# Optimization experiments

Measured on AMD Instinct MI355X. Metric: run time of the kernel, lower is better.

Reference implementation:

```python
import jax, jax.numpy as jnp
import numpy as np

B, T, C, H = 4, 2048, 1024, 16
D = C // H          # head_dim = 64
FF = 2 * C          # ff_mult = 2
EPS = 1e-5


def _layernorm(x, g, b):
    mu = jnp.mean(x, axis=-1, keepdims=True)
    var = jnp.mean((x - mu) ** 2, axis=-1, keepdims=True)
    return (x - mu) * jax.lax.rsqrt(var + EPS) * g + b


def setup_inputs() -> dict:
    key = jax.random.key(0)
    ks = jax.random.split(key, 8)
    x = jax.random.normal(ks[0], (B, T, C), dtype=jnp.float32)
    perm = jax.random.permutation(ks[1], T).astype(jnp.int32)
    s_c = 1.0 / np.sqrt(C)
    s_f = 1.0 / np.sqrt(FF)
    Wqkv = jax.random.normal(ks[2], (C, 3 * C), dtype=jnp.float32) * s_c
    Wproj = jax.random.normal(ks[3], (C, C), dtype=jnp.float32) * s_c
    bproj = jnp.zeros((C,), dtype=jnp.float32)
    ln1_g = jnp.ones((C,), dtype=jnp.float32)
    ln1_b = jnp.zeros((C,), dtype=jnp.float32)
    ln2_g = jnp.ones((C,), dtype=jnp.float32)
    ln2_b = jnp.zeros((C,), dtype=jnp.float32)
    Wff1 = jax.random.normal(ks[4], (C, FF), dtype=jnp.float32) * s_c
    bff1 = jnp.zeros((FF,), dtype=jnp.float32)
    Wff2 = jax.random.normal(ks[5], (FF, C), dtype=jnp.float32) * s_f
    bff2 = jnp.zeros((C,), dtype=jnp.float32)
    return {"x": x, "perm": perm, "Wqkv": Wqkv, "Wproj": Wproj, "bproj": bproj,
            "ln1_g": ln1_g, "ln1_b": ln1_b, "ln2_g": ln2_g, "ln2_b": ln2_b,
            "Wff1": Wff1, "bff1": bff1, "Wff2": Wff2, "bff2": bff2}


def reference(x, perm, Wqkv, Wproj, bproj, ln1_g, ln1_b, ln2_g, ln2_b,
              Wff1, bff1, Wff2, bff2):
    # --- attention branch ---
    h = _layernorm(x, ln1_g, ln1_b)                       # [B,T,C]
    qkv = (h @ Wqkv).reshape(B, T, 3, H, D)
    q, k, v = qkv[:, :, 0], qkv[:, :, 1], qkv[:, :, 2]    # [B,T,H,D]
    # random-permuted causal additive mask: masked = ~tril[:, perm]
    rows = jnp.arange(T)[:, None]
    masked = perm[None, :] > rows                          # [T,T] bool
    bias = jnp.where(masked, -jnp.inf, 0.0).astype(x.dtype)
    scale = 1.0 / np.sqrt(D)
    scores = jnp.einsum('bqhd,bkhd->bhqk', q, k) * scale + bias
    attn = jax.nn.softmax(scores, axis=-1)                 # [B,H,T,T]
    y = jnp.einsum('bhqk,bkhd->bqhd', attn, v).reshape(B, T, C)
    x = x + y @ Wproj + bproj
    # --- MLP branch ---
    h2 = _layernorm(x, ln2_g, ln2_b)
    ff = jax.nn.gelu(h2 @ Wff1 + bff1, approximate=False) @ Wff2 + bff2
    return x + ff
```

## Files before the change

### kernel.cpp

```cpp
#include <hip/hip_runtime.h>
#include <math.h>

#define Bb 4
#define Tt 2048
#define Cc 1024
#define Hh 16
#define Dd 64
#define FFf 2048
#define Mrows (Bb*Tt)

typedef _Float16 f16;
typedef _Float16 half8 __attribute__((ext_vector_type(8)));
typedef _Float16 half4 __attribute__((ext_vector_type(4)));
typedef _Float16 half2 __attribute__((ext_vector_type(2)));
typedef float floatx4 __attribute__((ext_vector_type(4)));
typedef float floatx16 __attribute__((ext_vector_type(16)));

#define MFMA16(a,b,c)    __builtin_amdgcn_mfma_f32_16x16x32_f16(a,b,c,0,0,0)
#define MFMA16K16(a,b,c) __builtin_amdgcn_mfma_f32_16x16x16f16(a,b,c,0,0,0)
#define MFMA32(a,b,c)    __builtin_amdgcn_mfma_f32_32x32x16_f16(a,b,c,0,0,0)

__device__ __forceinline__ void g2l16(const void* g, void* l) {
  __builtin_amdgcn_global_load_lds((__attribute__((address_space(1))) void*)(g),
                                   (__attribute__((address_space(3))) void*)(l),
                                   16, 0, 0);
}

__global__ __launch_bounds__(256) void wt_all_kernel(
    const float* __restrict__ Wqkv, const float* __restrict__ Wproj,
    const float* __restrict__ Wff1, const float* __restrict__ Wff2,
    f16* __restrict__ WqkvT, f16* __restrict__ WprojT,
    f16* __restrict__ Wff1T, f16* __restrict__ Wff2T) {
  __shared__ float tile[32][33];
  int idx = blockIdx.x;
  const float* W; f16* WT; int K, N, n0, k0;
  if (idx < 3072)      { W = Wqkv;  WT = WqkvT;  K = Cc;  N = 3*Cc; n0 = (idx % 96)*32; k0 = (idx / 96)*32; }
  else if (idx < 4096) { idx -= 3072; W = Wproj; WT = WprojT; K = Cc;  N = Cc;  n0 = (idx % 32)*32; k0 = (idx / 32)*32; }
  else if (idx < 6144) { idx -= 4096; W = Wff1;  WT = Wff1T;  K = Cc;  N = FFf; n0 = (idx % 64)*32; k0 = (idx / 64)*32; }
  else                 { idx -= 6144; W = Wff2;  WT = Wff2T;  K = FFf; N = Cc;  n0 = (idx % 32)*32; k0 = (idx / 32)*32; }
  const int tx = threadIdx.x, ty = threadIdx.y;
  #pragma unroll
  for (int i = 0; i < 4; i++)
    tile[ty + 8*i][tx] = W[(size_t)(k0 + ty + 8*i) * N + n0 + tx];
  __syncthreads();
  #pragma unroll
  for (int i = 0; i < 4; i++)
    WT[(size_t)(n0 + ty + 8*i) * K + k0 + tx] = (f16)tile[tx][ty + 8*i];
}

__global__ __launch_bounds__(256) void ln_kernel(const float* __restrict__ x,
                                                 const float* __restrict__ gam,
                                                 const float* __restrict__ bet,
                                                 f16* __restrict__ out) {
  const int row = blockIdx.x;
  const int tid = threadIdx.x;
  const float4 v = ((const float4*)(x + (size_t)row * Cc))[tid];
  float s  = v.x + v.y + v.z + v.w;
  float ss = v.x*v.x + v.y*v.y + v.z*v.z + v.w*v.w;
  #pragma unroll
  for (int o = 32; o >= 1; o >>= 1) { s += __shfl_xor(s, o); ss += __shfl_xor(ss, o); }
  __shared__ float ps[4], pss[4];
  if ((tid & 63) == 0) { ps[tid >> 6] = s; pss[tid >> 6] = ss; }
  __syncthreads();
  s  = ps[0] + ps[1] + ps[2] + ps[3];
  ss = pss[0] + pss[1] + pss[2] + pss[3];
  const float mu   = s * (1.0f / Cc);
  const float rstd = rsqrtf(ss * (1.0f / Cc) - mu * mu + 1e-5f);
  const float4 g4 = ((const float4*)gam)[tid];
  const float4 b4 = ((const float4*)bet)[tid];
  half4 o;
  o[0] = (f16)((v.x - mu) * rstd * g4.x + b4.x);
  o[1] = (f16)((v.y - mu) * rstd * g4.y + b4.y);
  o[2] = (f16)((v.z - mu) * rstd * g4.z + b4.z);
  o[3] = (f16)((v.w - mu) * rstd * g4.w + b4.w);
  ((half4*)(out + (size_t)row * Cc))[tid] = o;
}

template <int MODE>
__global__ __launch_bounds__(256, 3) void gemm_kernel(
    const f16* __restrict__ A, const f16* __restrict__ Bt, const int Kdim,
    const float* __restrict__ resid, const float* __restrict__ bias,
    float* __restrict__ outF, f16* __restrict__ outH,
    f16* __restrict__ outQ, f16* __restrict__ outK, f16* __restrict__ outV) {
  __shared__ f16 As[128 * 64];
  __shared__ f16 Bs[128 * 64];
  const int tid = threadIdx.x;
  const int lane = tid & 63;
  const int w = tid >> 6;
  const int wr = w >> 1, wc = w & 1;
  const int bm = blockIdx.y, bn = blockIdx.x;

  floatx16 acc[2][2] = {};

  const int srow = lane >> 3;
  const int scol = ((lane & 7) ^ srow) * 8;
  const size_t aBase = (size_t)(bm*128 + w*32 + srow) * Kdim + scol;
  const size_t bBase = (size_t)(bn*128 + w*32 + srow) * Kdim + scol;

  const int m0 = wr*64 + (lane & 31);
  const int n0 = wc*64 + (lane & 31);
  const int khalf = lane >> 5;
  const int mx = (lane & 7);

  for (int ks = 0; ks < Kdim; ks += 64) {
    __syncthreads();
    #pragma unroll
    for (int c = 0; c < 4; c++) {
      g2l16(A  + aBase + (size_t)(c*8)*Kdim + ks, &As[(w*32 + c*8) * 64]);
      g2l16(Bt + bBase + (size_t)(c*8)*Kdim + ks, &Bs[(w*32 + c*8) * 64]);
    }
    __syncthreads();
    #pragma unroll
    for (int kk = 0; kk < 4; kk++) {
      const int kg = kk*2 + khalf;
      half8 aF[2], bF[2];
      aF[0] = *(const half8*)&As[(m0     ) * 64 + ((kg ^ mx) * 8)];
      aF[1] = *(const half8*)&As[(m0 + 32) * 64 + ((kg ^ mx) * 8)];
      bF[0] = *(const half8*)&Bs[(n0     ) * 64 + ((kg ^ mx) * 8)];
      bF[1] = *(const half8*)&Bs[(n0 + 32) * 64 + ((kg ^ mx) * 8)];
      acc[0][0] = MFMA32(aF[0], bF[0], acc[0][0]);
      acc[0][1] = MFMA32(aF[0], bF[1], acc[0][1]);
      acc[1][0] = MFMA32(aF[1], bF[0], acc[1][0]);
      acc[1][1] = MFMA32(aF[1], bF[1], acc[1][1]);
    }
  }

  const int rowBase = bm*128 + wr*64;
  const int colBase = bn*128 + wc*64;
  #pragma unroll
  for (int mi = 0; mi < 2; mi++) {
    #pragma unroll
    for (int ni = 0; ni < 2; ni++) {
      const int col = colBase + ni*32 + (lane & 31);
      if (MODE == 0) {
        const int s = col >> 10;
        const int hh = (col >> 6) & 15;
        const int d = col & 63;
        #pragma unroll
        for (int g = 0; g < 4; g++) {
          const int row0 = rowBase + mi*32 + 4*khalf + 8*g;
          const int bI = row0 >> 11;
          const int t0 = row0 & 2047;
          if (s == 2) {
            const size_t addr = (((size_t)(bI*Hh + hh)) * Dd + d) * Tt +
                                (t0 & ~63) + ((t0 >> 2) & 3)*16 + ((t0 >> 4) & 3)*4;
            half4 o;
            #pragma unroll
            for (int r = 0; r < 4; r++) o[r] = (f16)acc[mi][ni][g*4 + r];
            *(half4*)&outV[addr] = o;
          } else {
            f16* dst = (s == 0) ? outQ : outK;
            const float sc = (s == 0) ? 0.18033688f : 1.0f;
            #pragma unroll
            for (int r = 0; r < 4; r++)
              dst[(((size_t)(bI*Hh + hh)) * Tt + t0 + r) * Dd + d] =
                  (f16)(acc[mi][ni][g*4 + r] * sc);
          }
        }
      } else {
        #pragma unroll
        for (int g = 0; g < 4; g++) {
          #pragma unroll
          for (int r = 0; r < 4; r++) {
            const int row = rowBase + mi*32 + 4*khalf + 8*g + r;
            const float vv = acc[mi][ni][g*4 + r];
            if (MODE == 1) {
              const size_t a = (size_t)row * Cc + col;
              outF[a] = vv + resid[a] + bias[col];
            } else if (MODE == 2) {
              const float t = vv + bias[col];
              const float gl = 0.5f * t * (1.0f + erff(t * 0.70710678118654752f));
              outH[(size_t)row * FFf + col] = (f16)gl;
            } else {
              const size_t a = (size_t)row * Cc + col;
              outF[a] = vv + bias[col] + resid[a];
            }
          }
        }
      }
    }
  }
}

__global__ __launch_bounds__(256, 4) void attn_kernel(
    const f16* __restrict__ Q, const f16* __restrict__ Kg,
    const f16* __restrict__ Vtp, const int* __restrict__ perm,
    f16* __restrict__ Y) {
  __shared__ f16 Ks[64 * 64];
  __shared__ f16 Vs[64 * 64];
  __shared__ int permS[64];

  const int tid = threadIdx.x;
  const int lane = tid & 63;
  const int w = tid >> 6;
  const int low = lane & 15;
  const int quad = lane >> 4;
  const int bh = blockIdx.y;
  const int q0 = blockIdx.x * 128;
  const int b = bh >> 4, h = bh & 15;

  half8 qF[2][2];
  {
    const size_t base = ((size_t)bh * Tt + q0 + w*32) * Dd;
    #pragma unroll
    for (int qi = 0; qi < 2; qi++)
      #pragma unroll
      for (int kc = 0; kc < 2; kc++)
        qF[qi][kc] = *(const half8*)(Q + base + (size_t)(qi*16 + low) * Dd +
                                     kc*32 + quad*8);
  }

  floatx4 O[4][2] = {};
  floatx4 Ol[2] = {};
  const half4 ones4 = {(f16)1.f, (f16)1.f, (f16)1.f, (f16)1.f};

  const int gd = ((lane & 7) ^ (lane >> 3)) * 8;
  const int krow = lane >> 3;

  for (int kt = 0; kt < Tt / 64; kt++) {
    const int kbase = kt * 64;
    __syncthreads();
    {
      const size_t kgBase = ((size_t)bh * Tt + kbase) * Dd;
      const size_t vgBase = ((size_t)bh * Dd) * Tt + kbase;
      g2l16(Kg  + kgBase + (size_t)(w*16 + 0 + krow) * Dd + gd, &Ks[(w*2 + 0) * 512]);
      g2l16(Kg  + kgBase + (size_t)(w*16 + 8 + krow) * Dd + gd, &Ks[(w*2 + 1) * 512]);
      g2l16(Vtp + vgBase + (size_t)(w*16 + 0 + krow) * Tt + gd, &Vs[(w*2 + 0) * 512]);
      g2l16(Vtp + vgBase + (size_t)(w*16 + 8 + krow) * Tt + gd, &Vs[(w*2 + 1) * 512]);
      if (tid < 64) permS[tid] = perm[kbase + tid];
    }
    __syncthreads();

    floatx4 S[2][4] = {};
    #pragma unroll
    for (int kc = 0; kc < 2; kc++) {
      #pragma unroll
      for (int ki = 0; ki < 4; ki++) {
        const int key = ki*16 + low;
        const half8 kf = *(const half8*)&Ks[key * 64 + (((kc*4 + quad) ^ (lane & 7)) * 8)];
        S[0][ki] = MFMA16(kf, qF[0][kc], S[0][ki]);
        S[1][ki] = MFMA16(kf, qF[1][kc], S[1][ki]);
      }
    }

    int4 pk[4];
    #pragma unroll
    for (int ki = 0; ki < 4; ki++) pk[ki] = *(const int4*)&permS[ki*16 + quad*4];

    half4 pF[2][4];
    #pragma unroll
    for (int qi = 0; qi < 2; qi++) {
      const int qrow = q0 + w*32 + qi*16 + low;
      #pragma unroll
      for (int ki = 0; ki < 4; ki++) {
        const floatx4 sv = S[qi][ki];
        const float p0 = (pk[ki].x > qrow) ? 0.f : __builtin_amdgcn_exp2f(sv[0]);
        const float p1 = (pk[ki].y > qrow) ? 0.f : __builtin_amdgcn_exp2f(sv[1]);
        const float p2 = (pk[ki].z > qrow) ? 0.f : __builtin_amdgcn_exp2f(sv[2]);
        const float p3 = (pk[ki].w > qrow) ? 0.f : __builtin_amdgcn_exp2f(sv[3]);
        const half2 lo = __builtin_bit_cast(half2, __builtin_amdgcn_cvt_pkrtz(p0, p1));
        const half2 hi = __builtin_bit_cast(half2, __builtin_amdgcn_cvt_pkrtz(p2, p3));
        pF[qi][ki] = __builtin_shufflevector(lo, hi, 0, 1, 2, 3);
      }
    }

    #pragma unroll
    for (int ki2 = 0; ki2 < 2; ki2++) {
      Ol[0] = MFMA16K16(ones4, pF[0][2*ki2 + 0], Ol[0]);
      Ol[1] = MFMA16K16(ones4, pF[1][2*ki2 + 0], Ol[1]);
      Ol[0] = MFMA16K16(ones4, pF[0][2*ki2 + 1], Ol[0]);
      Ol[1] = MFMA16K16(ones4, pF[1][2*ki2 + 1], Ol[1]);
      #pragma unroll
      for (int ni = 0; ni < 4; ni++) {
        const int d = ni*16 + low;
        const half8 v8 = *(const half8*)&Vs[d * 64 + (((quad*2 + ki2) ^ (lane & 7)) * 8)];
        const half4 vfA = __builtin_shufflevector(v8, v8, 0, 1, 2, 3);
        const half4 vfB = __builtin_shufflevector(v8, v8, 4, 5, 6, 7);
        O[ni][0] = MFMA16K16(vfA, pF[0][2*ki2 + 0], O[ni][0]);
        O[ni][1] = MFMA16K16(vfA, pF[1][2*ki2 + 0], O[ni][1]);
        O[ni][0] = MFMA16K16(vfB, pF[0][2*ki2 + 1], O[ni][0]);
        O[ni][1] = MFMA16K16(vfB, pF[1][2*ki2 + 1], O[ni][1]);
      }
    }
  }

  #pragma unroll
  for (int qi = 0; qi < 2; qi++) {
    const float linv = 1.0f / Ol[qi][0];
    const int trow = q0 + w*32 + qi*16 + low;
    #pragma unroll
    for (int ni = 0; ni < 4; ni++) {
      half4 o;
      #pragma unroll
      for (int r = 0; r < 4; r++) o[r] = (f16)(O[ni][qi][r] * linv);
      *(half4*)&Y[((size_t)(b * Tt + trow)) * Cc + h*64 + ni*16 + quad*4] = o;
    }
  }
}

extern "C" void kernel_launch(void* const* d_in, const int* in_sizes, int n_in,
                              void* d_out, int out_size, void* d_ws, size_t ws_size,
                              hipStream_t stream) {
  const float* x     = (const float*)d_in[0];
  const int*   perm  = (const int*)d_in[1];
  const float* Wqkv  = (const float*)d_in[2];
  const float* Wproj = (const float*)d_in[3];
  const float* bproj = (const float*)d_in[4];
  const float* ln1g  = (const float*)d_in[5];
  const float* ln1b  = (const float*)d_in[6];
  const float* ln2g  = (const float*)d_in[7];
  const float* ln2b  = (const float*)d_in[8];
  const float* Wff1  = (const float*)d_in[9];
  const float* bff1  = (const float*)d_in[10];
  const float* Wff2  = (const float*)d_in[11];
  const float* bff2  = (const float*)d_in[12];
  float* out = (float*)d_out;

  char* ws = (char*)d_ws;
  size_t off = 0;
  auto alloc = [&](size_t bytes) -> void* {
    void* p = ws + off;
    off += (bytes + 255) & ~(size_t)255;
    return p;
  };
  f16*   h1     = (f16*)alloc((size_t)Mrows * Cc * 2);
  f16*   qb     = (f16*)alloc((size_t)Mrows * Cc * 2);
  f16*   kb     = (f16*)alloc((size_t)Mrows * Cc * 2);
  f16*   vtp    = (f16*)alloc((size_t)Mrows * Cc * 2);
  f16*   yb     = (f16*)alloc((size_t)Mrows * Cc * 2);
  float* xa     = (float*)alloc((size_t)Mrows * Cc * 4);
  f16*   h2     = (f16*)alloc((size_t)Mrows * Cc * 2);
  f16*   gb     = (f16*)alloc((size_t)Mrows * FFf * 2);
  f16*   WqkvT  = (f16*)alloc((size_t)3 * Cc * Cc * 2);
  f16*   WprojT = (f16*)alloc((size_t)Cc * Cc * 2);
  f16*   Wff1T  = (f16*)alloc((size_t)FFf * Cc * 2);
  f16*   Wff2T  = (f16*)alloc((size_t)Cc * FFf * 2);

  wt_all_kernel<<<8192, dim3(32, 8), 0, stream>>>(Wqkv, Wproj, Wff1, Wff2,
                                                  WqkvT, WprojT, Wff1T, Wff2T);

  ln_kernel<<<Mrows, 256, 0, stream>>>(x, ln1g, ln1b, h1);

  gemm_kernel<0><<<dim3(3*Cc/128, Mrows/128), 256, 0, stream>>>(
      h1, WqkvT, Cc, nullptr, nullptr, nullptr, nullptr, qb, kb, vtp);

  attn_kernel<<<dim3(Tt/128, Bb*Hh), 256, 0, stream>>>(qb, kb, vtp, perm, yb);

  gemm_kernel<1><<<dim3(Cc/128, Mrows/128), 256, 0, stream>>>(
      yb, WprojT, Cc, x, bproj, xa, nullptr, nullptr, nullptr, nullptr);

  ln_kernel<<<Mrows, 256, 0, stream>>>(xa, ln2g, ln2b, h2);

  gemm_kernel<2><<<dim3(FFf/128, Mrows/128), 256, 0, stream>>>(
      h2, Wff1T, Cc, nullptr, bff1, nullptr, gb, nullptr, nullptr, nullptr);

  gemm_kernel<3><<<dim3(Cc/128, Mrows/128), 256, 0, stream>>>(
      gb, Wff2T, FFf, xa, bff2, out, nullptr, nullptr, nullptr, nullptr);
}
```

Before: 446.4 us.

## Double-buffer attention K/V tiles and raise GEMM occupancy bound

The attention kernel now keeps two LDS buffers for the K, V and perm tiles. It issues the async global-to-LDS load for the next key tile before computing on the current one, so each iteration needs one barrier instead of two and the load latency overlaps the MFMA work. The GEMM launch bound goes from 3 to 4 blocks per CU, and its epilogue moves into a separate inline helper. The costs are twice the LDS per attention block and tighter register limits on the GEMM, which could cause spills.

```diff
diff --git a/kernel.cpp b/kernel.cpp
--- a/kernel.cpp
+++ b/kernel.cpp
@@ -77,7 +77,60 @@
 }
 
 template <int MODE>
-__global__ __launch_bounds__(256, 3) void gemm_kernel(
+__device__ __forceinline__ void gemm_epilogue_tile(
+    const floatx16& a, int rowBase, int col, int khalf,
+    const float* __restrict__ resid, const float* __restrict__ bias,
+    float* __restrict__ outF, f16* __restrict__ outH,
+    f16* __restrict__ outQ, f16* __restrict__ outK, f16* __restrict__ outV) {
+  if (MODE == 0) {
+    const int s = col >> 10;
+    const int hh = (col >> 6) & 15;
+    const int d = col & 63;
+    #pragma unroll
+    for (int g = 0; g < 4; g++) {
+      const int row0 = rowBase + 4*khalf + 8*g;
+      const int bI = row0 >> 11;
+      const int t0 = row0 & 2047;
+      if (s == 2) {
+        const size_t addr = (((size_t)(bI*Hh + hh)) * Dd + d) * Tt +
+                            (t0 & ~63) + ((t0 >> 2) & 3)*16 + ((t0 >> 4) & 3)*4;
+        half4 o;
+        #pragma unroll
+        for (int r = 0; r < 4; r++) o[r] = (f16)a[g*4 + r];
+        *(half4*)&outV[addr] = o;
+      } else {
+        f16* dst = (s == 0) ? outQ : outK;
+        const float sc = (s == 0) ? 0.18033688f : 1.0f;
+        #pragma unroll
+        for (int r = 0; r < 4; r++)
+          dst[(((size_t)(bI*Hh + hh)) * Tt + t0 + r) * Dd + d] = (f16)(a[g*4 + r] * sc);
+      }
+    }
+  } else {
+    #pragma unroll
+    for (int g = 0; g < 4; g++) {
+      #pragma unroll
+      for (int r = 0; r < 4; r++) {
+        const int row = rowBase + 4*khalf + 8*g + r;
+        const float vv = a[g*4 + r];
+        if (MODE == 1) {
+          const size_t ad = (size_t)row * Cc + col;
+          outF[ad] = vv + resid[ad] + bias[col];
+        } else if (MODE == 2) {
+          const float t = vv + bias[col];
+          const float gl = 0.5f * t * (1.0f + erff(t * 0.70710678118654752f));
+          outH[(size_t)row * FFf + col] = (f16)gl;
+        } else {
+          const size_t ad = (size_t)row * Cc + col;
+          outF[ad] = vv + bias[col] + resid[ad];
+        }
+      }
+    }
+  }
+}
+
+template <int MODE>
+__global__ __launch_bounds__(256, 4) void gemm_kernel(
     const f16* __restrict__ A, const f16* __restrict__ Bt, const int Kdim,
     const float* __restrict__ resid, const float* __restrict__ bias,
     float* __restrict__ outF, f16* __restrict__ outH,
@@ -125,70 +178,22 @@
     }
   }
 
-  const int rowBase = bm*128 + wr*64;
-  const int colBase = bn*128 + wc*64;
-  #pragma unroll
-  for (int mi = 0; mi < 2; mi++) {
-    #pragma unroll
-    for (int ni = 0; ni < 2; ni++) {
-      const int col = colBase + ni*32 + (lane & 31);
-      if (MODE == 0) {
-        const int s = col >> 10;
-        const int hh = (col >> 6) & 15;
-        const int d = col & 63;
-        #pragma unroll
-        for (int g = 0; g < 4; g++) {
-          const int row0 = rowBase + mi*32 + 4*khalf + 8*g;
-          const int bI = row0 >> 11;
-          const int t0 = row0 & 2047;
-          if (s == 2) {
-            const size_t addr = (((size_t)(bI*Hh + hh)) * Dd + d) * Tt +
-                                (t0 & ~63) + ((t0 >> 2) & 3)*16 + ((t0 >> 4) & 3)*4;
-            half4 o;
-            #pragma unroll
-            for (int r = 0; r < 4; r++) o[r] = (f16)acc[mi][ni][g*4 + r];
-            *(half4*)&outV[addr] = o;
-          } else {
-            f16* dst = (s == 0) ? outQ : outK;
-            const float sc = (s == 0) ? 0.18033688f : 1.0f;
-            #pragma unroll
-            for (int r = 0; r < 4; r++)
-              dst[(((size_t)(bI*Hh + hh)) * Tt + t0 + r) * Dd + d] =
-                  (f16)(acc[mi][ni][g*4 + r] * sc);
-          }
-        }
-      } else {
-        #pragma unroll
-        for (int g = 0; g < 4; g++) {
-          #pragma unroll
-          for (int r = 0; r < 4; r++) {
-            const int row = rowBase + mi*32 + 4*khalf + 8*g + r;
-            const float vv = acc[mi][ni][g*4 + r];
-            if (MODE == 1) {
-              const size_t a = (size_t)row * Cc + col;
-              outF[a] = vv + resid[a] + bias[col];
-            } else if (MODE == 2) {
-              const float t = vv + bias[col];
-              const float gl = 0.5f * t * (1.0f + erff(t * 0.70710678118654752f));
-              outH[(size_t)row * FFf + col] = (f16)gl;
-            } else {
-              const size_t a = (size_t)row * Cc + col;
-              outF[a] = vv + bias[col] + resid[a];
-            }
-          }
-        }
-      }
-    }
-  }
+  #pragma unroll
+  for (int mi = 0; mi < 2; mi++)
+    #pragma unroll
+    for (int ni = 0; ni < 2; ni++)
+      gemm_epilogue_tile<MODE>(acc[mi][ni], blockIdx.y*128 + wr*64 + mi*32,
+                               blockIdx.x*128 + wc*64 + ni*32 + (lane & 31), khalf,
+                               resid, bias, outF, outH, outQ, outK, outV);
 }
 
 __global__ __launch_bounds__(256, 4) void attn_kernel(
     const f16* __restrict__ Q, const f16* __restrict__ Kg,
     const f16* __restrict__ Vtp, const int* __restrict__ perm,
     f16* __restrict__ Y) {
-  __shared__ f16 Ks[64 * 64];
-  __shared__ f16 Vs[64 * 64];
-  __shared__ int permS[64];
+  __shared__ f16 Ks[2 * 4096];
+  __shared__ f16 Vs[2 * 4096];
+  __shared__ int permS[2 * 64];
 
   const int tid = threadIdx.x;
   const int lane = tid & 63;
@@ -199,6 +204,21 @@
   const int q0 = blockIdx.x * 128;
   const int b = bh >> 4, h = bh & 15;
 
+  const int gd = ((lane & 7) ^ (lane >> 3)) * 8;
+  const int krow = lane >> 3;
+
+  const size_t kgBase0 = (size_t)bh * Tt * Dd;
+  const size_t vgBase0 = (size_t)bh * Dd * Tt;
+
+  auto stage = [&](int kt, int bufi) {
+    const int kbase = kt * 64;
+    g2l16(Kg  + kgBase0 + (size_t)(kbase + w*16 + 0 + krow) * Dd + gd, &Ks[bufi*4096 + (w*2 + 0) * 512]);
+    g2l16(Kg  + kgBase0 + (size_t)(kbase + w*16 + 8 + krow) * Dd + gd, &Ks[bufi*4096 + (w*2 + 1) * 512]);
+    g2l16(Vtp + vgBase0 + (size_t)(w*16 + 0 + krow) * Tt + kbase + gd, &Vs[bufi*4096 + (w*2 + 0) * 512]);
+    g2l16(Vtp + vgBase0 + (size_t)(w*16 + 8 + krow) * Tt + kbase + gd, &Vs[bufi*4096 + (w*2 + 1) * 512]);
+    if (tid < 64) permS[bufi*64 + tid] = perm[kbase + tid];
+  };
+
   half8 qF[2][2];
   {
     const size_t base = ((size_t)bh * Tt + q0 + w*32) * Dd;
@@ -214,22 +234,16 @@
   floatx4 Ol[2] = {};
   const half4 ones4 = {(f16)1.f, (f16)1.f, (f16)1.f, (f16)1.f};
 
-  const int gd = ((lane & 7) ^ (lane >> 3)) * 8;
-  const int krow = lane >> 3;
+  stage(0, 0);
 
   for (int kt = 0; kt < Tt / 64; kt++) {
-    const int kbase = kt * 64;
+    const int cur = kt & 1;
     __syncthreads();
-    {
-      const size_t kgBase = ((size_t)bh * Tt + kbase) * Dd;
-      const size_t vgBase = ((size_t)bh * Dd) * Tt + kbase;
-      g2l16(Kg  + kgBase + (size_t)(w*16 + 0 + krow) * Dd + gd, &Ks[(w*2 + 0) * 512]);
-      g2l16(Kg  + kgBase + (size_t)(w*16 + 8 + krow) * Dd + gd, &Ks[(w*2 + 1) * 512]);
-      g2l16(Vtp + vgBase + (size_t)(w*16 + 0 + krow) * Tt + gd, &Vs[(w*2 + 0) * 512]);
-      g2l16(Vtp + vgBase + (size_t)(w*16 + 8 + krow) * Tt + gd, &Vs[(w*2 + 1) * 512]);
-      if (tid < 64) permS[tid] = perm[kbase + tid];
-    }
-    __syncthreads();
+    if (kt + 1 < Tt / 64) stage(kt + 1, cur ^ 1);
+
+    const f16* KsH = &Ks[cur * 4096];
+    const f16* VsH = &Vs[cur * 4096];
+    const int* pS  = &permS[cur * 64];
 
     floatx4 S[2][4] = {};
     #pragma unroll
@@ -237,7 +251,7 @@
       #pragma unroll
       for (int ki = 0; ki < 4; ki++) {
         const int key = ki*16 + low;
-        const half8 kf = *(const half8*)&Ks[key * 64 + (((kc*4 + quad) ^ (lane & 7)) * 8)];
+        const half8 kf = *(const half8*)&KsH[key * 64 + (((kc*4 + quad) ^ (lane & 7)) * 8)];
         S[0][ki] = MFMA16(kf, qF[0][kc], S[0][ki]);
         S[1][ki] = MFMA16(kf, qF[1][kc], S[1][ki]);
       }
@@ -245,7 +259,7 @@
 
     int4 pk[4];
     #pragma unroll
-    for (int ki = 0; ki < 4; ki++) pk[ki] = *(const int4*)&permS[ki*16 + quad*4];
+    for (int ki = 0; ki < 4; ki++) pk[ki] = *(const int4*)&pS[ki*16 + quad*4];
 
     half4 pF[2][4];
     #pragma unroll
@@ -273,7 +287,7 @@
       #pragma unroll
       for (int ni = 0; ni < 4; ni++) {
         const int d = ni*16 + low;
-        const half8 v8 = *(const half8*)&Vs[d * 64 + (((quad*2 + ki2) ^ (lane & 7)) * 8)];
+        const half8 v8 = *(const half8*)&VsH[d * 64 + (((quad*2 + ki2) ^ (lane & 7)) * 8)];
         const half4 vfA = __builtin_shufflevector(v8, v8, 0, 1, 2, 3);
         const half4 vfB = __builtin_shufflevector(v8, v8, 4, 5, 6, 7);
         O[ni][0] = MFMA16K16(vfA, pF[0][2*ki2 + 0], O[ni][0]);
```

Result: no change. 448.4 us (+0.4%).

## Merge weight transpose with LN1, remap GEMM blocks per XCD, raise occupancy

Applied to the files above, without the earlier changes.

Folds the weight transpose/convert kernel and the first layernorm into a single launch, removing one kernel boundary. GEMM blocks are remapped so that each XCD (selected by fid&7) handles a fixed set of column tiles, which should improve L2 reuse of the B operand within each XCD. The GEMM launch bound is also raised from 3 to 4 waves, which may increase register pressure. The epilogue is moved into a helper without changing its behaviour.

```diff
diff --git a/kernel.cpp b/kernel.cpp
--- a/kernel.cpp
+++ b/kernel.cpp
@@ -26,26 +26,53 @@
                                    16, 0, 0);
 }
 
-__global__ __launch_bounds__(256) void wt_all_kernel(
+__global__ __launch_bounds__(256) void wt_ln_kernel(
     const float* __restrict__ Wqkv, const float* __restrict__ Wproj,
     const float* __restrict__ Wff1, const float* __restrict__ Wff2,
     f16* __restrict__ WqkvT, f16* __restrict__ WprojT,
-    f16* __restrict__ Wff1T, f16* __restrict__ Wff2T) {
-  __shared__ float tile[32][33];
-  int idx = blockIdx.x;
-  const float* W; f16* WT; int K, N, n0, k0;
-  if (idx < 3072)      { W = Wqkv;  WT = WqkvT;  K = Cc;  N = 3*Cc; n0 = (idx % 96)*32; k0 = (idx / 96)*32; }
-  else if (idx < 4096) { idx -= 3072; W = Wproj; WT = WprojT; K = Cc;  N = Cc;  n0 = (idx % 32)*32; k0 = (idx / 32)*32; }
-  else if (idx < 6144) { idx -= 4096; W = Wff1;  WT = Wff1T;  K = Cc;  N = FFf; n0 = (idx % 64)*32; k0 = (idx / 64)*32; }
-  else                 { idx -= 6144; W = Wff2;  WT = Wff2T;  K = FFf; N = Cc;  n0 = (idx % 32)*32; k0 = (idx / 32)*32; }
-  const int tx = threadIdx.x, ty = threadIdx.y;
-  #pragma unroll
-  for (int i = 0; i < 4; i++)
-    tile[ty + 8*i][tx] = W[(size_t)(k0 + ty + 8*i) * N + n0 + tx];
-  __syncthreads();
-  #pragma unroll
-  for (int i = 0; i < 4; i++)
-    WT[(size_t)(n0 + ty + 8*i) * K + k0 + tx] = (f16)tile[tx][ty + 8*i];
+    f16* __restrict__ Wff1T, f16* __restrict__ Wff2T,
+    const float* __restrict__ x, const float* __restrict__ gam,
+    const float* __restrict__ bet, f16* __restrict__ lnout) {
+  const int tid = threadIdx.x;
+  if (blockIdx.x < 8192) {
+    __shared__ float tile[32][33];
+    int idx = blockIdx.x;
+    const float* W; f16* WT; int K, N, n0, k0;
+    if (idx < 3072)      { W = Wqkv;  WT = WqkvT;  K = Cc;  N = 3*Cc; n0 = (idx % 96)*32; k0 = (idx / 96)*32; }
+    else if (idx < 4096) { idx -= 3072; W = Wproj; WT = WprojT; K = Cc;  N = Cc;  n0 = (idx % 32)*32; k0 = (idx / 32)*32; }
+    else if (idx < 6144) { idx -= 4096; W = Wff1;  WT = Wff1T;  K = Cc;  N = FFf; n0 = (idx % 64)*32; k0 = (idx / 64)*32; }
+    else                 { idx -= 6144; W = Wff2;  WT = Wff2T;  K = FFf; N = Cc;  n0 = (idx % 32)*32; k0 = (idx / 32)*32; }
+    const int tx = tid & 31, ty = tid >> 5;
+    #pragma unroll
+    for (int i = 0; i < 4; i++)
+      tile[ty + 8*i][tx] = W[(size_t)(k0 + ty + 8*i) * N + n0 + tx];
+    __syncthreads();
+    #pragma unroll
+    for (int i = 0; i < 4; i++)
+      WT[(size_t)(n0 + ty + 8*i) * K + k0 + tx] = (f16)tile[tx][ty + 8*i];
+  } else {
+    const int row = blockIdx.x - 8192;
+    const float4 v = ((const float4*)(x + (size_t)row * Cc))[tid];
+    float s  = v.x + v.y + v.z + v.w;
+    float ss = v.x*v.x + v.y*v.y + v.z*v.z + v.w*v.w;
+    #pragma unroll
+    for (int o = 32; o >= 1; o >>= 1) { s += __shfl_xor(s, o); ss += __shfl_xor(ss, o); }
+    __shared__ float ps[4], pss[4];
+    if ((tid & 63) == 0) { ps[tid >> 6] = s; pss[tid >> 6] = ss; }
+    __syncthreads();
+    s  = ps[0] + ps[1] + ps[2] + ps[3];
+    ss = pss[0] + pss[1] + pss[2] + pss[3];
+    const float mu   = s * (1.0f / Cc);
+    const float rstd = rsqrtf(ss * (1.0f / Cc) - mu * mu + 1e-5f);
+    const float4 g4 = ((const float4*)gam)[tid];
+    const float4 b4 = ((const float4*)bet)[tid];
+    half4 o;
+    o[0] = (f16)((v.x - mu) * rstd * g4.x + b4.x);
+    o[1] = (f16)((v.y - mu) * rstd * g4.y + b4.y);
+    o[2] = (f16)((v.z - mu) * rstd * g4.z + b4.z);
+    o[3] = (f16)((v.w - mu) * rstd * g4.w + b4.w);
+    ((half4*)(lnout + (size_t)row * Cc))[tid] = o;
+  }
 }
 
 __global__ __launch_bounds__(256) void ln_kernel(const float* __restrict__ x,
@@ -77,7 +104,60 @@
 }
 
 template <int MODE>
-__global__ __launch_bounds__(256, 3) void gemm_kernel(
+__device__ __forceinline__ void gemm_epilogue_tile(
+    const floatx16& a, int rowBase, int col, int khalf,
+    const float* __restrict__ resid, const float* __restrict__ bias,
+    float* __restrict__ outF, f16* __restrict__ outH,
+    f16* __restrict__ outQ, f16* __restrict__ outK, f16* __restrict__ outV) {
+  if (MODE == 0) {
+    const int s = col >> 10;
+    const int hh = (col >> 6) & 15;
+    const int d = col & 63;
+    #pragma unroll
+    for (int g = 0; g < 4; g++) {
+      const int row0 = rowBase + 4*khalf + 8*g;
+      const int bI = row0 >> 11;
+      const int t0 = row0 & 2047;
+      if (s == 2) {
+        const size_t addr = (((size_t)(bI*Hh + hh)) * Dd + d) * Tt +
+                            (t0 & ~63) + ((t0 >> 2) & 3)*16 + ((t0 >> 4) & 3)*4;
+        half4 o;
+        #pragma unroll
+        for (int r = 0; r < 4; r++) o[r] = (f16)a[g*4 + r];
+        *(half4*)&outV[addr] = o;
+      } else {
+        f16* dst = (s == 0) ? outQ : outK;
+        const float sc = (s == 0) ? 0.18033688f : 1.0f;
+        #pragma unroll
+        for (int r = 0; r < 4; r++)
+          dst[(((size_t)(bI*Hh + hh)) * Tt + t0 + r) * Dd + d] = (f16)(a[g*4 + r] * sc);
+      }
+    }
+  } else {
+    #pragma unroll
+    for (int g = 0; g < 4; g++) {
+      #pragma unroll
+      for (int r = 0; r < 4; r++) {
+        const int row = rowBase + 4*khalf + 8*g + r;
+        const float vv = a[g*4 + r];
+        if (MODE == 1) {
+          const size_t ad = (size_t)row * Cc + col;
+          outF[ad] = vv + resid[ad] + bias[col];
+        } else if (MODE == 2) {
+          const float t = vv + bias[col];
+          const float gl = 0.5f * t * (1.0f + erff(t * 0.70710678118654752f));
+          outH[(size_t)row * FFf + col] = (f16)gl;
+        } else {
+          const size_t ad = (size_t)row * Cc + col;
+          outF[ad] = vv + bias[col] + resid[ad];
+        }
+      }
+    }
+  }
+}
+
+template <int MODE>
+__global__ __launch_bounds__(256, 4) void gemm_kernel(
     const f16* __restrict__ A, const f16* __restrict__ Bt, const int Kdim,
     const float* __restrict__ resid, const float* __restrict__ bias,
     float* __restrict__ outF, f16* __restrict__ outH,
@@ -88,7 +168,13 @@
   const int lane = tid & 63;
   const int w = tid >> 6;
   const int wr = w >> 1, wc = w & 1;
-  const int bm = blockIdx.y, bn = blockIdx.x;
+
+  const int Mb = gridDim.y;
+  const int fid = blockIdx.y * gridDim.x + blockIdx.x;
+  const int xcd = fid & 7;
+  const int slot = fid >> 3;
+  const int bn = xcd + 8 * (slot / Mb);
+  const int bm = slot % Mb;
 
   floatx16 acc[2][2] = {};
 
@@ -125,61 +211,13 @@
     }
   }
 
-  const int rowBase = bm*128 + wr*64;
-  const int colBase = bn*128 + wc*64;
   #pragma unroll
-  for (int mi = 0; mi < 2; mi++) {
-    #pragma unroll
-    for (int ni = 0; ni < 2; ni++) {
-      const int col = colBase + ni*32 + (lane & 31);
-      if (MODE == 0) {
-        const int s = col >> 10;
-        const int hh = (col >> 6) & 15;
-        const int d = col & 63;
-        #pragma unroll
-        for (int g = 0; g < 4; g++) {
-          const int row0 = rowBase + mi*32 + 4*khalf + 8*g;
-          const int bI = row0 >> 11;
-          const int t0 = row0 & 2047;
-          if (s == 2) {
-            const size_t addr = (((size_t)(bI*Hh + hh)) * Dd + d) * Tt +
-                                (t0 & ~63) + ((t0 >> 2) & 3)*16 + ((t0 >> 4) & 3)*4;
-            half4 o;
-            #pragma unroll
-            for (int r = 0; r < 4; r++) o[r] = (f16)acc[mi][ni][g*4 + r];
-            *(half4*)&outV[addr] = o;
-          } else {
-            f16* dst = (s == 0) ? outQ : outK;
-            const float sc = (s == 0) ? 0.18033688f : 1.0f;
-            #pragma unroll
-            for (int r = 0; r < 4; r++)
-              dst[(((size_t)(bI*Hh + hh)) * Tt + t0 + r) * Dd + d] =
-                  (f16)(acc[mi][ni][g*4 + r] * sc);
-          }
-        }
-      } else {
-        #pragma unroll
-        for (int g = 0; g < 4; g++) {
-          #pragma unroll
-          for (int r = 0; r < 4; r++) {
-            const int row = rowBase + mi*32 + 4*khalf + 8*g + r;
-            const float vv = acc[mi][ni][g*4 + r];
-            if (MODE == 1) {
-              const size_t a = (size_t)row * Cc + col;
-              outF[a] = vv + resid[a] + bias[col];
-            } else if (MODE == 2) {
-              const float t = vv + bias[col];
-              const float gl = 0.5f * t * (1.0f + erff(t * 0.70710678118654752f));
-              outH[(size_t)row * FFf + col] = (f16)gl;
-            } else {
-              const size_t a = (size_t)row * Cc + col;
-              outF[a] = vv + bias[col] + resid[a];
-            }
-          }
-        }
-      }
-    }
-  }
+  for (int mi = 0; mi < 2; mi++)
+    #pragma unroll
+    for (int ni = 0; ni < 2; ni++)
+      gemm_epilogue_tile<MODE>(acc[mi][ni], bm*128 + wr*64 + mi*32,
+                               bn*128 + wc*64 + ni*32 + (lane & 31), khalf,
+                               resid, bias, outF, outH, outQ, outK, outV);
 }
 
 __global__ __launch_bounds__(256, 4) void attn_kernel(
@@ -336,10 +374,9 @@
   f16*   Wff1T  = (f16*)alloc((size_t)FFf * Cc * 2);
   f16*   Wff2T  = (f16*)alloc((size_t)Cc * FFf * 2);
 
-  wt_all_kernel<<<8192, dim3(32, 8), 0, stream>>>(Wqkv, Wproj, Wff1, Wff2,
-                                                  WqkvT, WprojT, Wff1T, Wff2T);
-
-  ln_kernel<<<Mrows, 256, 0, stream>>>(x, ln1g, ln1b, h1);
+  wt_ln_kernel<<<16384, 256, 0, stream>>>(Wqkv, Wproj, Wff1, Wff2,
+                                          WqkvT, WprojT, Wff1T, Wff2T,
+                                          x, ln1g, ln1b, h1);
 
   gemm_kernel<0><<<dim3(3*Cc/128, Mrows/128), 256, 0, stream>>>(
       h1, WqkvT, Cc, nullptr, nullptr, nullptr, nullptr, qb, kb, vtp);
```

Result: faster. 435.3 us (-2.5%).
